# Kernel tuning notes

Hardware: AMD Instinct MI355X
Metric: run time of the kernel (lower is better)

Reference implementation:

```python
import jax, jax.numpy as jnp
import numpy as np

IN_DIM = 1024
BS, NCROPS = 32, 1024


def setup_inputs() -> dict:
    key = jax.random.key(0)
    ks = jax.random.split(key, 7)
    s = 1.0 / np.sqrt(IN_DIM)
    return {
        "x": jax.random.normal(ks[0], (BS, NCROPS, IN_DIM), jnp.float32),
        "Wq": jax.random.uniform(ks[1], (IN_DIM,), jnp.float32, -s, s),
        "bq": jax.random.uniform(ks[2], (1,), jnp.float32, -s, s),
        "Wk": jax.random.uniform(ks[3], (IN_DIM,), jnp.float32, -s, s),
        "bk": jax.random.uniform(ks[4], (1,), jnp.float32, -s, s),
        "Wv": jax.random.uniform(ks[5], (IN_DIM, IN_DIM), jnp.float32, -s, s),
        "bv": jax.random.uniform(ks[6], (IN_DIM,), jnp.float32, -s, s),
    }


def reference(x, Wq, bq, Wk, bk, Wv, bv):
    # x: (bs, n, d). 1x1 Conv1d over permuted x == per-position linear maps.
    bs, n, d = x.shape
    q = jnp.einsum("bnd,d->bn", x, Wq) + bq  # (bs, n)   query_conv -> 1 channel
    k = jnp.einsum("bnd,d->bn", x, Wk) + bk  # (bs, n)   key_conv   -> 1 channel
    energy = q[:, :, None] * k[:, None, :]    # (bs, n, n) rank-1 outer product (bmm of (n,1)@(1,n))
    attention = jax.nn.softmax(energy, axis=-1)
    v = jnp.einsum("od,bnd->bon", Wv, x) + bv[None, :, None]  # (bs, d, n) value_conv
    out = jnp.einsum("bdn,bnm->bdm", v, attention)            # (bs, d, n)
    # Faithful to torch .view: raw reshape of (bs, d, n) -> (bs, n, d), NOT a transpose.
    out = out.reshape(bs, n, d)
    return (out, attention)
```

## Files before the change

### kernel.cpp

```cpp
#include <hip/hip_runtime.h>
#include <hip/hip_bf16.h>

#define BS  32
#define N   1024
#define DIM 1024

typedef unsigned short u16;
typedef unsigned int   u32;

typedef __attribute__((ext_vector_type(8))) __bf16 bf16x8;
typedef __attribute__((ext_vector_type(4))) float  f32x4;

__device__ __forceinline__ u16 f2bf(float f) {
    u32 u = __builtin_bit_cast(u32, f);
    u = (u + 0x7FFF + ((u >> 16) & 1)) >> 16;
    return (u16)u;
}

__device__ __forceinline__ void async16(const u16* g, u16* l) {
    __builtin_amdgcn_global_load_lds(
        (const __attribute__((address_space(1))) u32*)g,
        (__attribute__((address_space(3))) u32*)l,
        16, 0, 0);
}

__global__ void convert_qk(const float* __restrict__ x,
                           const float* __restrict__ Wq, const float* __restrict__ bq,
                           const float* __restrict__ Wk, const float* __restrict__ bk,
                           const float* __restrict__ Wv,
                           u16* __restrict__ xb, u16* __restrict__ Wvb,
                           float* __restrict__ qv, float* __restrict__ kv)
{
    int gw   = (blockIdx.x * 256 + threadIdx.x) >> 6;
    int lane = threadIdx.x & 63;
    bool isX = gw < BS * N;
    const float* src = isX ? (x + (size_t)gw * DIM) : (Wv + (size_t)(gw - BS * N) * DIM);
    u16*         dst = isX ? (xb + (size_t)gw * DIM) : (Wvb + (size_t)(gw - BS * N) * DIM);
    float qd = 0.f, kd = 0.f;
    #pragma unroll
    for (int i = 0; i < 4; ++i) {
        int e = i * 256 + lane * 4;
        float4 xv = *(const float4*)&src[e];
        uint2 p;
        p.x = (u32)f2bf(xv.x) | ((u32)f2bf(xv.y) << 16);
        p.y = (u32)f2bf(xv.z) | ((u32)f2bf(xv.w) << 16);
        *(uint2*)&dst[e] = p;
        if (isX) {
            float4 wq = *(const float4*)&Wq[e];
            float4 wk = *(const float4*)&Wk[e];
            qd += xv.x * wq.x + xv.y * wq.y + xv.z * wq.z + xv.w * wq.w;
            kd += xv.x * wk.x + xv.y * wk.y + xv.z * wk.z + xv.w * wk.w;
        }
    }
    if (isX) {
        #pragma unroll
        for (int off = 32; off; off >>= 1) {
            qd += __shfl_xor(qd, off);
            kd += __shfl_xor(kd, off);
        }
        if (lane == 0) { qv[gw] = qd + bq[0]; kv[gw] = kd + bk[0]; }
    }
}

__global__ void zker(const float* __restrict__ qv, const float* __restrict__ kv,
                     float* __restrict__ invZ)
{
    int gw   = (blockIdx.x * 256 + threadIdx.x) >> 6;
    int lane = threadIdx.x & 63;
    int b    = gw >> 10;
    float qi = qv[gw];
    const float* kr = kv + (size_t)b * N;
    float z = 0.f;
    #pragma unroll
    for (int i = 0; i < 4; ++i) {
        int e = i * 256 + lane * 4;
        float4 kk = *(const float4*)&kr[e];
        z += __expf(qi * kk.x) + __expf(qi * kk.y) + __expf(qi * kk.z) + __expf(qi * kk.w);
    }
    #pragma unroll
    for (int off = 32; off; off >>= 1) z += __shfl_xor(z, off);
    if (lane == 0) invZ[gw] = 1.0f / z;
}

__global__ void attker(const float* __restrict__ qv, const float* __restrict__ kv,
                       const float* __restrict__ invZ,
                       float* __restrict__ att, u16* __restrict__ aT)
{
    int bid = blockIdx.x;
    int b   = bid >> 8;
    int t   = bid & 255;
    int i0  = (t >> 4) * 64, j0 = (t & 15) * 64;
    __shared__ float sq[64], siz[64], sk[64];
    int tid = threadIdx.x;
    if (tid < 64)        sq[tid]        = qv[b * N + i0 + tid];
    else if (tid < 128)  siz[tid - 64]  = invZ[b * N + i0 + (tid - 64)];
    else if (tid < 192)  sk[tid - 128]  = kv[b * N + j0 + (tid - 128)];
    __syncthreads();
    float* ab = att + (size_t)b * N * N;
    u16*   tb = aT  + (size_t)b * N * N;
    #pragma unroll 4
    for (int s = 0; s < 16; ++s) {
        int idx = s * 256 + tid;
        int r = idx >> 6, c = idx & 63;
        float a = __expf(sq[r] * sk[c]) * siz[r];
        ab[(size_t)(i0 + r) * N + j0 + c] = a;
    }
    #pragma unroll 4
    for (int s = 0; s < 16; ++s) {
        int idx = s * 256 + tid;
        int c = idx >> 6, r = idx & 63;
        float a = __expf(sq[r] * sk[c]) * siz[r];
        tb[(size_t)(j0 + c) * N + i0 + r] = f2bf(a);
    }
}

template<int BF16OUT, int BIAS>
__global__ __launch_bounds__(256) void gemm_bt(
    const u16* __restrict__ A, size_t aBatch,
    const u16* __restrict__ B, size_t bBatch,
    void* __restrict__ C, size_t cBatch,
    const float* __restrict__ bias)
{
    const int K = 1024, LD = 1024;
    int blk = blockIdx.x;
    int b   = blk >> 6;
    int t   = blk & 63;
    int m0  = (t >> 3) * 128, n0 = (t & 7) * 128;
    const u16* Ab = A + aBatch * (size_t)b;
    const u16* Bb = B + bBatch * (size_t)b;
    __shared__ u16 lA[128 * 32];
    __shared__ u16 lB[128 * 32];
    int w = threadIdx.x >> 6, lane = threadIdx.x & 63;
    int wr = (w >> 1) * 64, wc = (w & 1) * 64;
    int rowl = lane >> 2;
    int col8 = (lane & 3) * 8;
    int frow = lane & 15, fk = (lane >> 4) * 8;
    f32x4 acc[4][4] = {};

    for (int k0 = 0; k0 < K; k0 += 32) {
        #pragma unroll
        for (int s = 0; s < 2; ++s) {
            int rr = (s * 4 + w) * 16;
            const u16* ga = Ab + (size_t)(m0 + rr + rowl) * LD + k0 + col8;
            const u16* gb = Bb + (size_t)(n0 + rr + rowl) * LD + k0 + col8;
            async16(ga, &lA[rr * 32]);
            async16(gb, &lB[rr * 32]);
        }
        __syncthreads();
        bf16x8 af[4], bfr[4];
        #pragma unroll
        for (int i = 0; i < 4; ++i)
            af[i] = *(const bf16x8*)&lA[(wr + i * 16 + frow) * 32 + fk];
        #pragma unroll
        for (int j = 0; j < 4; ++j)
            bfr[j] = *(const bf16x8*)&lB[(wc + j * 16 + frow) * 32 + fk];
        #pragma unroll
        for (int i = 0; i < 4; ++i)
            #pragma unroll
            for (int j = 0; j < 4; ++j)
                acc[i][j] = __builtin_amdgcn_mfma_f32_16x16x32_bf16(af[i], bfr[j], acc[i][j], 0, 0, 0);
        __syncthreads();
    }

    int r4 = (lane >> 4) * 4, cc = lane & 15;
    #pragma unroll
    for (int i = 0; i < 4; ++i) {
        #pragma unroll
        for (int j = 0; j < 4; ++j) {
            #pragma unroll
            for (int rg = 0; rg < 4; ++rg) {
                int row = m0 + wr + i * 16 + r4 + rg;
                int col = n0 + wc + j * 16 + cc;
                float v = acc[i][j][rg];
                if (BIAS) v += bias[row];
                if (BF16OUT)
                    ((u16*)C + cBatch * (size_t)b)[(size_t)row * LD + col] = f2bf(v);
                else
                    ((float*)C + cBatch * (size_t)b)[(size_t)row * LD + col] = v;
            }
        }
    }
}

extern "C" void kernel_launch(void* const* d_in, const int* in_sizes, int n_in,
                              void* d_out, int out_size, void* d_ws, size_t ws_size,
                              hipStream_t stream)
{
    const float* x  = (const float*)d_in[0];
    const float* Wq = (const float*)d_in[1];
    const float* bq = (const float*)d_in[2];
    const float* Wk = (const float*)d_in[3];
    const float* bk = (const float*)d_in[4];
    const float* Wv = (const float*)d_in[5];
    const float* bv = (const float*)d_in[6];

    float* out = (float*)d_out;
    float* att = out + (size_t)BS * N * N;

    char* ws = (char*)d_ws;
    u16*  xb   = (u16*)ws;
    u16*  vb   = xb + (size_t)BS * N * DIM;
    u16*  aT   = vb + (size_t)BS * N * DIM;
    u16*  Wvb  = aT + (size_t)BS * N * N;
    float* qv  = (float*)(Wvb + (size_t)DIM * DIM);
    float* kv  = qv + BS * N;
    float* invZ = kv + BS * N;

    convert_qk<<<(BS * N + DIM) / 4, 256, 0, stream>>>(x, Wq, bq, Wk, bk, Wv, xb, Wvb, qv, kv);
    zker<<<(BS * N) / 4, 256, 0, stream>>>(qv, kv, invZ);
    attker<<<BS * 256, 256, 0, stream>>>(qv, kv, invZ, att, aT);
    gemm_bt<1, 1><<<BS * 64, 256, 0, stream>>>(Wvb, 0, xb, (size_t)N * DIM, vb, (size_t)N * DIM, bv);
    gemm_bt<0, 0><<<BS * 64, 256, 0, stream>>>(vb, (size_t)N * DIM, aT, (size_t)N * N, out, (size_t)N * N, nullptr);
}
```

Before: 631.3 us.

## Fuse attention recomputation into second GEMM and merge softmax normalizer into row writer

Drops the separate bf16 transposed attention buffer. The second GEMM now recomputes exp(q_k*k_n)*invZ on the fly as its B operand from a per-batch (q, invZ) table held in shared memory. The normalizer pass and the fp32 attention write are merged into one row-wise kernel that writes with float4 stores. Block-to-batch mapping is also swizzled across 8 groups. This removes a 64 MB bf16 write and read plus one launch, at the cost of extra exp work inside the GEMM main loop.

```diff
diff --git a/kernel.cpp b/kernel.cpp
--- a/kernel.cpp
+++ b/kernel.cpp
@@ -62,71 +62,58 @@
     }
 }
 
-__global__ void zker(const float* __restrict__ qv, const float* __restrict__ kv,
-                     float* __restrict__ invZ)
-{
-    int gw   = (blockIdx.x * 256 + threadIdx.x) >> 6;
-    int lane = threadIdx.x & 63;
-    int b    = gw >> 10;
-    float qi = qv[gw];
-    const float* kr = kv + (size_t)b * N;
+__global__ void att_writer(const float* __restrict__ qv, const float* __restrict__ kvg,
+                           float* __restrict__ att, float2* __restrict__ qzg)
+{
+    int blk = blockIdx.x;
+    int b   = blk >> 6;
+    int r0  = (blk & 63) * 16;
+    __shared__ float ks[1024];
+    int tid = threadIdx.x;
+    #pragma unroll
+    for (int i = 0; i < 4; ++i) ks[i * 256 + tid] = kvg[b * N + i * 256 + tid];
+    int row = tid >> 4;
+    int c16 = tid & 15;
+    float qrow = qv[b * N + r0 + row];
+    __syncthreads();
     float z = 0.f;
-    #pragma unroll
-    for (int i = 0; i < 4; ++i) {
-        int e = i * 256 + lane * 4;
-        float4 kk = *(const float4*)&kr[e];
-        z += __expf(qi * kk.x) + __expf(qi * kk.y) + __expf(qi * kk.z) + __expf(qi * kk.w);
-    }
-    #pragma unroll
-    for (int off = 32; off; off >>= 1) z += __shfl_xor(z, off);
-    if (lane == 0) invZ[gw] = 1.0f / z;
-}
-
-__global__ void attker(const float* __restrict__ qv, const float* __restrict__ kv,
-                       const float* __restrict__ invZ,
-                       float* __restrict__ att, u16* __restrict__ aT)
-{
-    int bid = blockIdx.x;
-    int b   = bid >> 8;
-    int t   = bid & 255;
-    int i0  = (t >> 4) * 64, j0 = (t & 15) * 64;
-    __shared__ float sq[64], siz[64], sk[64];
-    int tid = threadIdx.x;
-    if (tid < 64)        sq[tid]        = qv[b * N + i0 + tid];
-    else if (tid < 128)  siz[tid - 64]  = invZ[b * N + i0 + (tid - 64)];
-    else if (tid < 192)  sk[tid - 128]  = kv[b * N + j0 + (tid - 128)];
-    __syncthreads();
-    float* ab = att + (size_t)b * N * N;
-    u16*   tb = aT  + (size_t)b * N * N;
     #pragma unroll 4
     for (int s = 0; s < 16; ++s) {
-        int idx = s * 256 + tid;
-        int r = idx >> 6, c = idx & 63;
-        float a = __expf(sq[r] * sk[c]) * siz[r];
-        ab[(size_t)(i0 + r) * N + j0 + c] = a;
-    }
+        const float4 kk = *(const float4*)&ks[(c16 + s * 16) * 4];
+        z += __expf(qrow * kk.x) + __expf(qrow * kk.y)
+           + __expf(qrow * kk.z) + __expf(qrow * kk.w);
+    }
+    z += __shfl_xor(z, 1); z += __shfl_xor(z, 2);
+    z += __shfl_xor(z, 4); z += __shfl_xor(z, 8);
+    float invZ = 1.0f / z;
+    if (c16 == 0) qzg[b * N + r0 + row] = make_float2(qrow, invZ);
+    float* ab = att + (size_t)b * N * N + (size_t)(r0 + row) * N;
     #pragma unroll 4
     for (int s = 0; s < 16; ++s) {
-        int idx = s * 256 + tid;
-        int c = idx >> 6, r = idx & 63;
-        float a = __expf(sq[r] * sk[c]) * siz[r];
-        tb[(size_t)(j0 + c) * N + i0 + r] = f2bf(a);
-    }
-}
-
-template<int BF16OUT, int BIAS>
+        int c0 = (c16 + s * 16) * 4;
+        const float4 kk = *(const float4*)&ks[c0];
+        float4 o;
+        o.x = __expf(qrow * kk.x) * invZ;
+        o.y = __expf(qrow * kk.y) * invZ;
+        o.z = __expf(qrow * kk.z) * invZ;
+        o.w = __expf(qrow * kk.w) * invZ;
+        *(float4*)&ab[c0] = o;
+    }
+}
+
 __global__ __launch_bounds__(256) void gemm_bt(
-    const u16* __restrict__ A, size_t aBatch,
+    const u16* __restrict__ A,
     const u16* __restrict__ B, size_t bBatch,
-    void* __restrict__ C, size_t cBatch,
+    u16* __restrict__ C, size_t cBatch,
     const float* __restrict__ bias)
 {
     const int K = 1024, LD = 1024;
-    int blk = blockIdx.x;
-    int b   = blk >> 6;
-    int t   = blk & 63;
+    int blk  = blockIdx.x;
+    int rest = blk >> 3;
+    int b    = (blk & 7) * 4 + (rest >> 6);
+    int t    = rest & 63;
     int m0  = (t >> 3) * 128, n0 = (t & 7) * 128;
-    const u16* Ab = A + aBatch * (size_t)b;
+    const u16* Ab = A;
     const u16* Bb = B + bBatch * (size_t)b;
     __shared__ u16 lA[128 * 32];
     __shared__ u16 lB[128 * 32];
@@ -141,10 +128,8 @@
         #pragma unroll
         for (int s = 0; s < 2; ++s) {
             int rr = (s * 4 + w) * 16;
-            const u16* ga = Ab + (size_t)(m0 + rr + rowl) * LD + k0 + col8;
-            const u16* gb = Bb + (size_t)(n0 + rr + rowl) * LD + k0 + col8;
-            async16(ga, &lA[rr * 32]);
-            async16(gb, &lB[rr * 32]);
+            async16(Ab + (size_t)(m0 + rr + rowl) * LD + k0 + col8, &lA[rr * 32]);
+            async16(Bb + (size_t)(n0 + rr + rowl) * LD + k0 + col8, &lB[rr * 32]);
         }
         __syncthreads();
         bf16x8 af[4], bfr[4];
@@ -163,23 +148,97 @@
     }
 
     int r4 = (lane >> 4) * 4, cc = lane & 15;
-    #pragma unroll
-    for (int i = 0; i < 4; ++i) {
-        #pragma unroll
-        for (int j = 0; j < 4; ++j) {
+    u16* Cb = C + cBatch * (size_t)b;
+    #pragma unroll
+    for (int i = 0; i < 4; ++i)
+        #pragma unroll
+        for (int j = 0; j < 4; ++j)
             #pragma unroll
             for (int rg = 0; rg < 4; ++rg) {
                 int row = m0 + wr + i * 16 + r4 + rg;
                 int col = n0 + wc + j * 16 + cc;
-                float v = acc[i][j][rg];
-                if (BIAS) v += bias[row];
-                if (BF16OUT)
-                    ((u16*)C + cBatch * (size_t)b)[(size_t)row * LD + col] = f2bf(v);
-                else
-                    ((float*)C + cBatch * (size_t)b)[(size_t)row * LD + col] = v;
+                Cb[(size_t)row * LD + col] = f2bf(acc[i][j][rg] + bias[row]);
             }
-        }
-    }
+}
+
+__global__ __launch_bounds__(256) void gemm2_fused(
+    const u16* __restrict__ A,
+    const float2* __restrict__ qzg,
+    const float* __restrict__ kvg,
+    float* __restrict__ C)
+{
+    const int K = 1024, LD = 1024;
+    int blk  = blockIdx.x;
+    int rest = blk >> 3;
+    int b    = (blk & 7) * 4 + (rest >> 6);
+    int t    = rest & 63;
+    int m0  = (t >> 3) * 128, n0 = (t & 7) * 128;
+    const u16* Ab = A + (size_t)b * K * LD;
+    __shared__ u16   lA[128 * 32];
+    __shared__ float2 qz[1024];
+    int tid = threadIdx.x;
+    int w = tid >> 6, lane = tid & 63;
+    int wr = (w >> 1) * 64, wc = (w & 1) * 64;
+    int rowl = lane >> 2;
+    int col8 = (lane & 3) * 8;
+    int frow = lane & 15, fk = (lane >> 4) * 8;
+
+    const float2* qzb = qzg + (size_t)b * N;
+    #pragma unroll
+    for (int i = 0; i < 4; ++i) qz[i * 256 + tid] = qzb[i * 256 + tid];
+    float kk[4];
+    #pragma unroll
+    for (int j = 0; j < 4; ++j) kk[j] = kvg[(size_t)b * N + n0 + wc + j * 16 + frow];
+    f32x4 acc[4][4] = {};
+    __syncthreads();
+
+    for (int k0 = 0; k0 < K; k0 += 32) {
+        #pragma unroll
+        for (int s = 0; s < 2; ++s) {
+            int rr = (s * 4 + w) * 16;
+            async16(Ab + (size_t)(m0 + rr + rowl) * LD + k0 + col8, &lA[rr * 32]);
+        }
+        const float4* qsrc = (const float4*)&qz[k0 + fk];
+        float4 qp[4];
+        #pragma unroll
+        for (int u = 0; u < 4; ++u) qp[u] = qsrc[u];
+        bf16x8 bfr[4];
+        #pragma unroll
+        for (int j = 0; j < 4; ++j) {
+            union { u32 u[4]; bf16x8 v; } pk;
+            #pragma unroll
+            for (int u = 0; u < 4; ++u) {
+                float e0 = __expf(qp[u].x * kk[j]) * qp[u].y;
+                float e1 = __expf(qp[u].z * kk[j]) * qp[u].w;
+                pk.u[u] = (u32)f2bf(e0) | ((u32)f2bf(e1) << 16);
+            }
+            bfr[j] = pk.v;
+        }
+        __syncthreads();
+        bf16x8 af[4];
+        #pragma unroll
+        for (int i = 0; i < 4; ++i)
+            af[i] = *(const bf16x8*)&lA[(wr + i * 16 + frow) * 32 + fk];
+        #pragma unroll
+        for (int i = 0; i < 4; ++i)
+            #pragma unroll
+            for (int j = 0; j < 4; ++j)
+                acc[i][j] = __builtin_amdgcn_mfma_f32_16x16x32_bf16(af[i], bfr[j], acc[i][j], 0, 0, 0);
+        __syncthreads();
+    }
+
+    int r4 = (lane >> 4) * 4, cc = lane & 15;
+    float* Cb = C + (size_t)b * K * LD;
+    #pragma unroll
+    for (int i = 0; i < 4; ++i)
+        #pragma unroll
+        for (int j = 0; j < 4; ++j)
+            #pragma unroll
+            for (int rg = 0; rg < 4; ++rg) {
+                int row = m0 + wr + i * 16 + r4 + rg;
+                int col = n0 + wc + j * 16 + cc;
+                Cb[(size_t)row * LD + col] = acc[i][j][rg];
+            }
 }
 
 extern "C" void kernel_launch(void* const* d_in, const int* in_sizes, int n_in,
@@ -200,15 +259,13 @@
     char* ws = (char*)d_ws;
     u16*  xb   = (u16*)ws;
     u16*  vb   = xb + (size_t)BS * N * DIM;
-    u16*  aT   = vb + (size_t)BS * N * DIM;
-    u16*  Wvb  = aT + (size_t)BS * N * N;
+    u16*  Wvb  = vb + (size_t)BS * N * DIM;
     float* qv  = (float*)(Wvb + (size_t)DIM * DIM);
     float* kv  = qv + BS * N;
-    float* invZ = kv + BS * N;
+    float2* qzg = (float2*)(kv + BS * N);
 
     convert_qk<<<(BS * N + DIM) / 4, 256, 0, stream>>>(x, Wq, bq, Wk, bk, Wv, xb, Wvb, qv, kv);
-    zker<<<(BS * N) / 4, 256, 0, stream>>>(qv, kv, invZ);
-    attker<<<BS * 256, 256, 0, stream>>>(qv, kv, invZ, att, aT);
-    gemm_bt<1, 1><<<BS * 64, 256, 0, stream>>>(Wvb, 0, xb, (size_t)N * DIM, vb, (size_t)N * DIM, bv);
-    gemm_bt<0, 0><<<BS * 64, 256, 0, stream>>>(vb, (size_t)N * DIM, aT, (size_t)N * N, out, (size_t)N * N, nullptr);
-}
+    att_writer<<<BS * 64, 256, 0, stream>>>(qv, kv, att, qzg);
+    gemm_bt<<<BS * 64, 256, 0, stream>>>(Wvb, xb, (size_t)N * DIM, vb, (size_t)N * DIM, bv);
+    gemm2_fused<<<BS * 64, 256, 0, stream>>>(vb, qzg, kv, out);
+}
```

Result: faster. 596.0 us (-5.6%).
